# Kernel tuning notes

Measured on AMD Instinct MI355X. Metric: run time of the kernel, lower is better.

The kernel has to match this reference:

```python
import jax, jax.numpy as jnp
import numpy as np

D_MODEL = 512
D_STATE = 128
D_CONV = 4
EXPAND = 2
HEADDIM = 64
D_INNER = EXPAND * D_MODEL            # 1024
NHEADS = D_INNER // HEADDIM           # 16
CONV_DIM = D_INNER + 2 * D_STATE      # 1280
D_IN_PROJ = 2 * D_INNER + 2 * D_STATE + NHEADS  # 2320
EPS = 1e-5


def _mamba2(u, in_w, conv_w, conv_b, A_log, dt_bias, Dp, norm_w, out_w):
    # u: [b, l, d_model]  -- Mamba2 forward (ngroups=1), SSD in exact quadratic form
    b, l, _ = u.shape
    zxbcdt = u @ in_w.T                                   # [b,l,2320]
    z = zxbcdt[..., :D_INNER]
    xBC = zxbcdt[..., D_INNER:D_INNER + CONV_DIM]
    dt = zxbcdt[..., D_INNER + CONV_DIM:]                 # [b,l,nheads]
    # causal depthwise conv1d (kernel 4) + silu
    xp = jnp.pad(xBC, ((0, 0), (D_CONV - 1, 0), (0, 0)))
    conv = sum(xp[:, k:k + l, :] * conv_w[:, k] for k in range(D_CONV))
    xBC = jax.nn.silu(conv + conv_b)
    x = xBC[..., :D_INNER].reshape(b, l, NHEADS, HEADDIM)
    Bm = xBC[..., D_INNER:D_INNER + D_STATE]              # [b,l,d_state]
    Cm = xBC[..., D_INNER + D_STATE:]                     # [b,l,d_state]
    dt = jax.nn.softplus(dt + dt_bias)                    # [b,l,nheads]
    dtA = dt * (-jnp.exp(A_log))                          # [b,l,nheads], negative
    # SSD quadratic (semiseparable) form: L[t,s] = exp(sum_{r=s+1..t} dtA_r), causal
    cs = jnp.cumsum(dtA, axis=1)                          # [b,l,nh]
    seg = cs[:, :, None, :] - cs[:, None, :, :]           # [b,t,s,nh]
    mask = jnp.tril(jnp.ones((l, l), bool))
    L = jnp.exp(jnp.where(mask[None, :, :, None], seg, -jnp.inf))
    G = jnp.einsum('btd,bsd->bts', Cm, Bm)                # C_t . B_s
    dtx = dt[..., None] * x                               # [b,l,nh,hd]
    y = jnp.einsum('btsn,bsnp->btnp', G[..., None] * L, dtx)
    y = (y + x * Dp[:, None]).reshape(b, l, D_INNER)      # D skip
    # gated RMSNorm (norm_before_gate=False): rmsnorm(y * silu(z)) * weight
    y = y * jax.nn.silu(z)
    y = y * jax.lax.rsqrt(jnp.mean(jnp.square(y), -1, keepdims=True) + EPS) * norm_w
    return y @ out_w.T


def _forward(x, h_in_w, h_conv_w, h_conv_b, h_A_log, h_dt_bias, h_D, h_norm_w, h_out_w,
             v_in_w, v_conv_w, v_conv_b, v_A_log, v_dt_bias, v_D, v_norm_w, v_out_w,
             fc_w, fc_b):
    B, H, W, C = x.shape
    hp = (h_in_w, h_conv_w, h_conv_b, h_A_log, h_dt_bias, h_D, h_norm_w, h_out_w)
    vp = (v_in_w, v_conv_w, v_conv_b, v_A_log, v_dt_bias, v_D, v_norm_w, v_out_w)
    # horizontal: scan along W for each (B*H) row
    xh = x.reshape(-1, W, C)
    h1 = _mamba2(xh, *hp)
    # NOTE: original code flips dim 0 (batch), reproduced faithfully
    h2 = jnp.flip(_mamba2(jnp.flip(xh, 0), *hp), 0)
    h = jnp.concatenate([h1, h2], -1).reshape(B, H, W, -1)
    # vertical: scan along H for each (B*W) column
    xv = jnp.transpose(x, (0, 2, 1, 3)).reshape(-1, H, C)
    v1 = _mamba2(xv, *vp)
    v2 = jnp.flip(_mamba2(jnp.flip(xv, 0), *vp), 0)
    v = jnp.transpose(jnp.concatenate([v1, v2], -1).reshape(B, W, H, -1), (0, 2, 1, 3))
    out = jnp.concatenate([v, h], -1) @ fc_w.T + fc_b     # [B,H,W,C]
    return out


def setup_inputs() -> dict:
    key = jax.random.key(0)
    ks = jax.random.split(key, 8)
    B, H, W, C = 2, 64, 64, D_MODEL
    x = jax.random.normal(ks[0], (B, H, W, C), jnp.float32)

    def mk(k):
        kk = jax.random.split(k, 5)
        return {
            'in_w': 0.02 * jax.random.normal(kk[0], (D_IN_PROJ, D_MODEL), jnp.float32),
            'conv_w': 0.1 * jax.random.normal(kk[1], (CONV_DIM, D_CONV), jnp.float32),
            'conv_b': jnp.zeros((CONV_DIM,), jnp.float32),
            'A_log': jnp.log(jax.random.uniform(kk[2], (NHEADS,), jnp.float32, 1.0, 16.0)),
            'dt_bias': jnp.log(jnp.expm1(jax.random.uniform(kk[3], (NHEADS,), jnp.float32, 1e-3, 0.1))),
            'D': jnp.ones((NHEADS,), jnp.float32),
            'norm_w': jnp.ones((D_INNER,), jnp.float32),
            'out_w': 0.02 * jax.random.normal(kk[4], (D_MODEL, D_INNER), jnp.float32),
        }

    hp, vp = mk(ks[1]), mk(ks[2])
    inp = {'x': x}
    inp.update({f'h_{n}': v for n, v in hp.items()})
    inp.update({f'v_{n}': v for n, v in vp.items()})
    inp['fc_w'] = 0.02 * jax.random.normal(ks[3], (D_MODEL, 4 * D_MODEL), jnp.float32)
    inp['fc_b'] = jnp.zeros((D_MODEL,), jnp.float32)
    return inp


def reference(x, h_in_w, h_conv_w, h_conv_b, h_A_log, h_dt_bias, h_D, h_norm_w, h_out_w,
              v_in_w, v_conv_w, v_conv_b, v_A_log, v_dt_bias, v_D, v_norm_w, v_out_w,
              fc_w, fc_b):
    return _forward(x, h_in_w, h_conv_w, h_conv_b, h_A_log, h_dt_bias, h_D, h_norm_w, h_out_w,
                    v_in_w, v_conv_w, v_conv_b, v_A_log, v_dt_bias, v_D, v_norm_w, v_out_w,
                    fc_w, fc_b)
```

## Files before the change

### kernel.cpp

```cpp
#include <hip/hip_runtime.h>

#define NROWS 8192
#define NZX   2304
#define BCS   136
#define XMS   72

#define PB0 4096
#define PB1 (PB0 + 2048)
#define PB2 (PB1 + 2304)
#define PB3 (PB2 + 256)
#define PB4 (PB3 + 512)

typedef __attribute__((ext_vector_type(8))) short bf16x8;
typedef __attribute__((ext_vector_type(4))) float f32x4;

__device__ __forceinline__ float bf2f(unsigned short u) {
    union { unsigned int i; float f; } v; v.i = ((unsigned int)u) << 16; return v.f;
}
__device__ __forceinline__ unsigned short f2bf(float f) {
    union { float f; unsigned int i; } v; v.f = f;
    return (unsigned short)((v.i + 0x8000u) >> 16);
}

__device__ __forceinline__ void async_lds16(const unsigned short* g, unsigned short* l) {
    __builtin_amdgcn_global_load_lds(
        (const __attribute__((address_space(1))) unsigned int*)g,
        (__attribute__((address_space(3))) unsigned int*)l, 16, 0, 0);
}

__global__ __launch_bounds__(256) void prep_kernel(
    const float* __restrict__ x, const float* __restrict__ fcw,
    const float* __restrict__ iw0, const float* __restrict__ iw1,
    const float* __restrict__ ow0, const float* __restrict__ ow1,
    const float* __restrict__ db0, const float* __restrict__ db1,
    const float* __restrict__ al0, const float* __restrict__ al1,
    unsigned short* __restrict__ xbf, unsigned short* __restrict__ wf,
    unsigned short* __restrict__ wbA, unsigned short* __restrict__ wbOT0,
    unsigned short* __restrict__ wbOT1, float* __restrict__ dtbb,
    float* __restrict__ csbb)
{
    __shared__ char sm[37888] __attribute__((aligned(16)));
    const int blk = blockIdx.x, tid = threadIdx.x;
    if (blk < PB0) {
        int i = blk * 256 + tid;
        float4 v = *(const float4*)(x + (size_t)i * 4);
        ushort4 o;
        o.x = f2bf(v.x); o.y = f2bf(v.y); o.z = f2bf(v.z); o.w = f2bf(v.w);
        *(ushort4*)(xbf + (size_t)i * 4) = o;
    } else if (blk < PB1) {
        int idx = (blk - PB0) * 256 + tid;
        int o = idx >> 10, c = idx & 1023;
        int half = c >> 9, cc = c & 511;
        float v = fcw[(size_t)o * 2048 + half * 1024 + cc] +
                  fcw[(size_t)o * 2048 + half * 1024 + 512 + cc];
        wf[idx] = f2bf(v);
    } else if (blk < PB2) {
        int local = blk - PB1;
        int dir = local / 1152;
        int i = (local % 1152) * 256 + tid;
        const float* s = dir ? iw1 : iw0;
        float4 v = *(const float4*)(s + (size_t)i * 4);
        ushort4 o;
        o.x = f2bf(v.x); o.y = f2bf(v.y); o.z = f2bf(v.z); o.w = f2bf(v.w);
        *(ushort4*)(wbA + (size_t)dir * (2304 * 512) + (size_t)i * 4) = o;
    } else if (blk < PB3) {
        float (*T)[65] = (float(*)[65])sm;
        int local = blk - PB2;
        int z = local >> 7, rem = local & 127;
        const float* s = z ? ow1 : ow0;
        unsigned short* d = z ? wbOT1 : wbOT0;
        const int bo = (rem >> 4) * 64, bc = (rem & 15) * 64;
#pragma unroll
        for (int i = 0; i < 16; ++i) {
            int slot = tid + i * 256;
            int r = slot >> 6, c = slot & 63;
            T[r][c] = s[(size_t)(bo + r) * 1024 + bc + c];
        }
        __syncthreads();
#pragma unroll
        for (int i = 0; i < 16; ++i) {
            int slot = tid + i * 256;
            int cr = slot >> 6, oc = slot & 63;
            d[(size_t)(bc + cr) * 512 + bo + oc] = f2bf(T[oc][cr]);
        }
    } else {
        float (*wsm)[512] = (float(*)[512])sm;
        float (*xs)[68]   = (float(*)[68])(sm + 16384);
        float (*dta)[64]  = (float(*)[64])(sm + 16384 + 17408);
        float (*dtt)[64]  = (float(*)[64])(sm + 16384 + 17408 + 2048);
        int local = blk - PB3;
        const int dir = local >> 8, bxl = local & 255;
        const float* in_w = dir ? iw1 : iw0;
        const float* dt_bias = dir ? db1 : db0;
        const float* A_log = dir ? al1 : al0;
        float* dtb = dtbb + (size_t)dir * 131072;
        float* csb = csbb + (size_t)dir * 131072;
        const int seq = bxl >> 1, hq = bxl & 1;
#pragma unroll
        for (int i = 0; i < 4; ++i) {
            int slot = tid + i * 256;
            int h = slot >> 7, c = (slot & 127) * 4;
            *(float4*)&wsm[h][c] = *(const float4*)(in_w + (size_t)(2304 + hq * 8 + h) * 512 + c);
        }
        const int t = tid & 63, hg = tid >> 6;
        float acc[2] = {0.f, 0.f};
        for (int c0 = 0; c0 < 512; c0 += 64) {
            __syncthreads();
#pragma unroll
            for (int i = 0; i < 4; ++i) {
                int slot = tid + i * 256;
                int r = slot >> 4, cc = (slot & 15) * 4;
                size_t row = (dir == 0) ? (size_t)seq * 64 + r
                                        : (size_t)(seq >> 6) * 4096 + (size_t)r * 64 + (seq & 63);
                *(float4*)&xs[r][cc] = *(const float4*)(x + row * 512 + c0 + cc);
            }
            __syncthreads();
#pragma unroll
            for (int cc = 0; cc < 64; cc += 4) {
                float4 u4 = *(const float4*)&xs[t][cc];
                const float* w0 = &wsm[hg * 2][c0 + cc];
                const float* w1 = &wsm[hg * 2 + 1][c0 + cc];
                acc[0] += u4.x * w0[0] + u4.y * w0[1] + u4.z * w0[2] + u4.w * w0[3];
                acc[1] += u4.x * w1[0] + u4.y * w1[1] + u4.z * w1[2] + u4.w * w1[3];
            }
        }
#pragma unroll
        for (int hh = 0; hh < 2; ++hh) {
            int hl = hg * 2 + hh;
            int h = hq * 8 + hl;
            float v = acc[hh] + dt_bias[h];
            float dtv = (v > 20.f) ? v : log1pf(__expf(v));
            dtt[hl][t] = dtv;
            dta[hl][t] = dtv * -__expf(A_log[h]);
        }
        __syncthreads();
        if (tid < 8) {
            float run = 0.f;
            int ob = (seq * 16 + hq * 8 + tid) * 64;
            for (int tt = 0; tt < 64; ++tt) {
                run += dta[tid][tt];
                dtb[ob + tt] = dtt[tid][tt];
                csb[ob + tt] = run;
            }
        }
    }
}

__global__ __launch_bounds__(256) void gemm_phase(
    const unsigned short* __restrict__ xbf, const unsigned short* __restrict__ wbA,
    unsigned short* __restrict__ zx, const unsigned short* __restrict__ wf,
    const unsigned short* __restrict__ wbOT0, const unsigned short* __restrict__ wbOT1,
    unsigned short* __restrict__ wcomb)
{
    __shared__ unsigned short SMEM[16384];
    unsigned short* As = SMEM;
    unsigned short* Bs = SMEM + 8192;
    const int bx = blockIdx.x, by = blockIdx.y, z = blockIdx.z;
    const unsigned short *A, *B;
    unsigned short* C;
    int lda, ldb, ldc, perm, mB, nB;
    if (bx < 64) {
        A = xbf; lda = 512; perm = z;
        B = wbA + (size_t)z * (2304 * 512); ldb = 512;
        C = zx + (size_t)z * NROWS * NZX; ldc = NZX;
        mB = bx * 128; nB = by * 128;
    } else {
        if (by >= 8) return;
        A = z ? wf : wf + 512; lda = 1024; perm = 0;
        B = z ? wbOT1 : wbOT0; ldb = 512;
        C = z ? wcomb : wcomb + 1024; ldc = 2048;
        mB = (bx - 64) * 128; nB = by * 128;
    }
    const int tid = threadIdx.x, wave = tid >> 6, lane = tid & 63;
    const int wm = (wave >> 1) * 64, wn = (wave & 1) * 64;
    const int lr = lane & 15, lq = lane >> 4;
    const unsigned short* AgP[4];
    const unsigned short* BgP[4];
    unsigned short* lA[4];
    unsigned short* lB[4];
#pragma unroll
    for (int i = 0; i < 4; ++i) {
        int s = tid + i * 256;
        int r = s >> 3, p = s & 7;
        int q = p ^ (r & 7);
        int ar = mB + r;
        if (perm) ar = (ar & ~4095) | ((ar & 63) << 6) | ((ar >> 6) & 63);
        AgP[i] = A + (size_t)ar * lda + q * 8;
        BgP[i] = B + (size_t)(nB + r) * ldb + q * 8;
        lA[i] = As + s * 8;
        lB[i] = Bs + s * 8;
    }
    const int aswz = lr & 7;
    int arb[4], brb[4];
#pragma unroll
    for (int i = 0; i < 4; ++i) {
        arb[i] = (wm + i * 16 + lr) * 64;
        brb[i] = (wn + i * 16 + lr) * 64;
    }
    f32x4 zero4 = {0.f,0.f,0.f,0.f};
    f32x4 acc[4][4] = {{zero4,zero4,zero4,zero4},{zero4,zero4,zero4,zero4},
                       {zero4,zero4,zero4,zero4},{zero4,zero4,zero4,zero4}};
    for (int k0 = 0; k0 < 512; k0 += 64) {
#pragma unroll
        for (int i = 0; i < 4; ++i) async_lds16(AgP[i] + k0, lA[i]);
#pragma unroll
        for (int i = 0; i < 4; ++i) async_lds16(BgP[i] + k0, lB[i]);
        __syncthreads();
#pragma unroll
        for (int kh = 0; kh < 2; ++kh) {
            const int ksw = ((kh * 4 + lq) ^ aswz) * 8;
            bf16x8 a[4], b[4];
#pragma unroll
            for (int i = 0; i < 4; ++i) a[i] = *(const bf16x8*)(As + arb[i] + ksw);
#pragma unroll
            for (int i = 0; i < 4; ++i) b[i] = *(const bf16x8*)(Bs + brb[i] + ksw);
#pragma unroll
            for (int mi = 0; mi < 4; ++mi)
#pragma unroll
                for (int ni = 0; ni < 4; ++ni)
                    acc[mi][ni] = __builtin_amdgcn_mfma_f32_16x16x32_bf16(
                        a[mi], b[ni], acc[mi][ni], 0, 0, 0);
        }
        __syncthreads();
    }
    unsigned short* WR = SMEM + wave * 1024;
#pragma unroll
    for (int mi = 0; mi < 4; ++mi) {
#pragma unroll
        for (int ni = 0; ni < 4; ++ni) {
#pragma unroll
            for (int r = 0; r < 4; ++r) {
                int r16 = lq * 4 + r;
                int cn = ni * 16 + lr;
                int gp = ((cn >> 3) + (r16 >> 1)) & 7;
                WR[r16 * 64 + gp * 8 + (cn & 7)] = f2bf(acc[mi][ni][r]);
            }
        }
#pragma unroll
        for (int j = 0; j < 2; ++j) {
            int r16 = j * 8 + (lane >> 3);
            int gr = lane & 7;
            int gp = (gr + (r16 >> 1)) & 7;
            uint4 v = *(const uint4*)(WR + r16 * 64 + gp * 8);
            int row = mB + wm + mi * 16 + r16;
            *(uint4*)(C + (size_t)row * ldc + nB + wn + gr * 8) = v;
        }
    }
}

__global__ __launch_bounds__(256) void gemm_final2048(
    const unsigned short* __restrict__ YV, const unsigned short* __restrict__ YH,
    const unsigned short* __restrict__ W, const float* __restrict__ bias,
    float* __restrict__ C)
{
    __shared__ unsigned short As[128 * 64];
    __shared__ unsigned short Bs[64 * 64];
    const int tid = threadIdx.x, wave = tid >> 6, lane = tid & 63;
    const int mB = blockIdx.x * 128, nB = blockIdx.y * 64;
    const int lr = lane & 15, lq = lane >> 4;
    int aq[4], agr[4], apr[4];
    unsigned short* lA[4];
    const unsigned short* BgP[2];
    unsigned short* lB[2];
#pragma unroll
    for (int i = 0; i < 4; ++i) {
        int s = tid + i * 256;
        int r = s >> 3, p = s & 7;
        aq[i] = (p ^ (r & 7)) * 8;
        int gr = mB + r;
        agr[i] = gr;
        apr[i] = (gr & ~4095) | ((gr & 63) << 6) | ((gr >> 6) & 63);
        lA[i] = As + s * 8;
    }
#pragma unroll
    for (int i = 0; i < 2; ++i) {
        int s = tid + i * 256;
        int r = s >> 3, p = s & 7;
        int q = p ^ (r & 7);
        BgP[i] = W + (size_t)(nB + r) * 2048 + q * 8;
        lB[i] = Bs + s * 8;
    }
    const int aswz = lr & 7;
    int arb[2], brb[4];
#pragma unroll
    for (int i = 0; i < 2; ++i) arb[i] = (wave * 32 + i * 16 + lr) * 64;
#pragma unroll
    for (int i = 0; i < 4; ++i) brb[i] = (i * 16 + lr) * 64;
    f32x4 zero4 = {0.f,0.f,0.f,0.f};
    f32x4 acc[2][4] = {{zero4,zero4,zero4,zero4},{zero4,zero4,zero4,zero4}};
    for (int k0 = 0; k0 < 2048; k0 += 64) {
#pragma unroll
        for (int i = 0; i < 4; ++i) {
            int kk = k0 + aq[i];
            const unsigned short* g = (kk < 1024)
                ? YV + (size_t)apr[i] * 1024 + kk
                : YH + (size_t)agr[i] * 1024 + (kk - 1024);
            async_lds16(g, lA[i]);
        }
#pragma unroll
        for (int i = 0; i < 2; ++i) async_lds16(BgP[i] + k0, lB[i]);
        __syncthreads();
#pragma unroll
        for (int kh = 0; kh < 2; ++kh) {
            const int ksw = ((kh * 4 + lq) ^ aswz) * 8;
            bf16x8 a[2], b[4];
#pragma unroll
            for (int i = 0; i < 2; ++i) a[i] = *(const bf16x8*)(As + arb[i] + ksw);
#pragma unroll
            for (int i = 0; i < 4; ++i) b[i] = *(const bf16x8*)(Bs + brb[i] + ksw);
#pragma unroll
            for (int mi = 0; mi < 2; ++mi)
#pragma unroll
                for (int ni = 0; ni < 4; ++ni)
                    acc[mi][ni] = __builtin_amdgcn_mfma_f32_16x16x32_bf16(
                        a[mi], b[ni], acc[mi][ni], 0, 0, 0);
        }
        __syncthreads();
    }
    const int rbase = lq * 4;
#pragma unroll
    for (int mi = 0; mi < 2; ++mi)
#pragma unroll
        for (int ni = 0; ni < 4; ++ni) {
            int col = nB + ni * 16 + lr;
            float bb = bias[col];
#pragma unroll
            for (int r = 0; r < 4; ++r) {
                int row = mB + wave * 32 + mi * 16 + rbase + r;
                C[(size_t)row * 512 + col] = acc[mi][ni][r] + bb;
            }
        }
}

__global__ __launch_bounds__(320) void conv_silu(
    const unsigned short* __restrict__ zxb, const float* __restrict__ cw0,
    const float* __restrict__ cw1, const float* __restrict__ cb0,
    const float* __restrict__ cb1, unsigned short* __restrict__ xbcb)
{
    __shared__ unsigned short S[64 * 320];
    const int dir = blockIdx.y;
    const unsigned short* zx = zxb + (size_t)dir * NROWS * NZX;
    unsigned short* xbc = xbcb + (size_t)dir * NROWS * 1280;
    const float* cw = dir ? cw1 : cw0;
    const float* cb = dir ? cb1 : cb0;
    const int tid = threadIdx.x;
    const int seq = blockIdx.x >> 2, tile = blockIdx.x & 3;
    const int cbase = tile * 320;
    const unsigned short* src = zx + (size_t)seq * 64 * NZX + 1024 + cbase;
#pragma unroll
    for (int i = 0; i < 8; ++i) {
        int slot = tid + i * 320;
        int r = slot / 40, ch = (slot % 40) * 8;
        *(uint4*)(S + r * 320 + ch) = *(const uint4*)(src + (size_t)r * NZX + ch);
    }
    __syncthreads();
    const int c8 = (tid % 40) * 8, rg = tid / 40;
    const int gc = cbase + c8;
    float4 b0 = *(const float4*)(cb + gc), b1 = *(const float4*)(cb + gc + 4);
    const float bias[8] = {b0.x,b0.y,b0.z,b0.w,b1.x,b1.y,b1.z,b1.w};
    float4 wv[8];
#pragma unroll
    for (int j = 0; j < 8; ++j) wv[j] = *(const float4*)(cw + (size_t)(gc + j) * 4);
    unsigned short* dst = xbc + (size_t)seq * 64 * 1280 + gc;
#pragma unroll
    for (int r = 0; r < 8; ++r) {
        int t = rg * 8 + r;
        float acc[8];
#pragma unroll
        for (int j = 0; j < 8; ++j) acc[j] = bias[j];
#pragma unroll
        for (int k = 0; k < 4; ++k) {
            int ts = t + k - 3;
            if (ts >= 0) {
                uint4 xv = *(const uint4*)(S + ts * 320 + c8);
                const unsigned short* xs = (const unsigned short*)&xv;
#pragma unroll
                for (int j = 0; j < 8; ++j)
                    acc[j] += bf2f(xs[j]) * ((const float*)&wv[j])[k];
            }
        }
        unsigned short out8[8] __attribute__((aligned(16)));
#pragma unroll
        for (int j = 0; j < 8; ++j) out8[j] = f2bf(acc[j] / (1.f + __expf(-acc[j])));
        *(uint4*)(dst + (size_t)t * 1280) = *(const uint4*)out8;
    }
}

__global__ __launch_bounds__(256) void scan_kernel(
    const unsigned short* __restrict__ xbcb, const float* __restrict__ dtbb,
    const float* __restrict__ csbb, const float* __restrict__ Dv0,
    const float* __restrict__ Dv1, unsigned short* __restrict__ yh,
    unsigned short* __restrict__ yv)
{
    __shared__ unsigned short Bs[64 * BCS];
    __shared__ unsigned short Cs[64 * BCS];
    __shared__ unsigned short XsT[64 * XMS];
    __shared__ unsigned short Ms[64 * XMS];
    __shared__ float dts[64], css[64];
    const int dir = blockIdx.y;
    const unsigned short* xbc = xbcb + (size_t)dir * NROWS * 1280;
    const float* dtb = dtbb + (size_t)dir * 131072;
    const float* csb = csbb + (size_t)dir * 131072;
    const float* Dv = dir ? Dv1 : Dv0;
    unsigned short* y = dir ? yv : yh;
    const int tid = threadIdx.x;
    const int lane = tid & 63, wave = tid >> 6;
    const int seq = blockIdx.x >> 4, h = blockIdx.x & 15;
    if (tid < 64) {
        dts[tid] = dtb[(seq * 16 + h) * 64 + tid];
        css[tid] = csb[(seq * 16 + h) * 64 + tid];
    }
    const unsigned short* base = xbc + (size_t)seq * 64 * 1280;
#pragma unroll
    for (int i = 0; i < 4; ++i) {
        int e = (tid + i * 256) * 8;
        int r = e >> 7, c = e & 127;
        *(uint4*)(Bs + r * BCS + c) = *(const uint4*)(base + (size_t)r * 1280 + 1024 + c);
        *(uint4*)(Cs + r * BCS + c) = *(const uint4*)(base + (size_t)r * 1280 + 1152 + c);
    }
#pragma unroll
    for (int i = 0; i < 2; ++i) {
        int e = (tid + i * 256) * 8;
        int t = e >> 6, p0 = e & 63;
        uint4 xval = *(const uint4*)(base + (size_t)t * 1280 + h * 64 + p0);
        const unsigned short* xs = (const unsigned short*)&xval;
#pragma unroll
        for (int j = 0; j < 8; ++j) {
            int jl = (j + lane) & 7;
            XsT[(p0 + jl) * XMS + t] = xs[jl];
        }
    }
    __syncthreads();
    const int lr = lane & 15, lq = lane >> 4;
    f32x4 zero4 = {0.f,0.f,0.f,0.f};
    f32x4 acc[4] = {zero4, zero4, zero4, zero4};
#pragma unroll
    for (int kt = 0; kt < 4; ++kt) {
        bf16x8 a = *(const bf16x8*)(Cs + (wave * 16 + lr) * BCS + kt * 32 + lq * 8);
#pragma unroll
        for (int ni = 0; ni < 4; ++ni) {
            bf16x8 b = *(const bf16x8*)(Bs + (ni * 16 + lr) * BCS + kt * 32 + lq * 8);
            acc[ni] = __builtin_amdgcn_mfma_f32_16x16x32_bf16(a, b, acc[ni], 0, 0, 0);
        }
    }
    float css_t[4];
#pragma unroll
    for (int r = 0; r < 4; ++r) css_t[r] = css[wave * 16 + lq * 4 + r];
#pragma unroll
    for (int ni = 0; ni < 4; ++ni) {
        int s = ni * 16 + lr;
        float cs_s = css[s], dt_s = dts[s];
#pragma unroll
        for (int r = 0; r < 4; ++r) {
            int t = wave * 16 + lq * 4 + r;
            float e = __expf(fminf(css_t[r] - cs_s, 0.f));
            float m = (s <= t) ? acc[ni][r] * e * dt_s : 0.f;
            Ms[t * XMS + s] = f2bf(m);
        }
    }
    __syncthreads();
    f32x4 yacc[4] = {zero4, zero4, zero4, zero4};
#pragma unroll
    for (int kt = 0; kt < 2; ++kt) {
        bf16x8 a = *(const bf16x8*)(Ms + (wave * 16 + lr) * XMS + kt * 32 + lq * 8);
#pragma unroll
        for (int ni = 0; ni < 4; ++ni) {
            bf16x8 b = *(const bf16x8*)(XsT + (ni * 16 + lr) * XMS + kt * 32 + lq * 8);
            yacc[ni] = __builtin_amdgcn_mfma_f32_16x16x32_bf16(a, b, yacc[ni], 0, 0, 0);
        }
    }
    const float Dh = Dv[h];
#pragma unroll
    for (int ni = 0; ni < 4; ++ni) {
        int p = ni * 16 + lr;
#pragma unroll
        for (int r = 0; r < 4; ++r) {
            int t = wave * 16 + lq * 4 + r;
            float v = yacc[ni][r] + Dh * bf2f(XsT[p * XMS + t]);
            Ms[t * XMS + p] = f2bf(v);
        }
    }
    __syncthreads();
    unsigned short* yout = y + (size_t)seq * 64 * 1024 + h * 64;
#pragma unroll
    for (int i = 0; i < 2; ++i) {
        int slot = tid + i * 256;
        int t = slot >> 3, pc = (slot & 7) * 8;
        uint4 v = *(const uint4*)(Ms + t * XMS + pc);
        *(uint4*)(yout + (size_t)t * 1024 + pc) = v;
    }
}

__global__ __launch_bounds__(128) void gate_norm(
    const unsigned short* __restrict__ zxb, unsigned short* __restrict__ yh,
    unsigned short* __restrict__ yv, const float* __restrict__ nw0,
    const float* __restrict__ nw1)
{
    const int dir = blockIdx.y;
    const unsigned short* zx = zxb + (size_t)dir * NROWS * NZX;
    unsigned short* y = dir ? yv : yh;
    const float* nw = dir ? nw1 : nw0;
    const int row = blockIdx.x, tid = threadIdx.x;
    uint4 yv4 = *(const uint4*)(y + (size_t)row * 1024 + tid * 8);
    uint4 zv4 = *(const uint4*)(zx + (size_t)row * NZX + tid * 8);
    const unsigned short* ys = (const unsigned short*)&yv4;
    const unsigned short* zs = (const unsigned short*)&zv4;
    float g[8]; float ss = 0.f;
#pragma unroll
    for (int j = 0; j < 8; ++j) {
        float zv = bf2f(zs[j]);
        float gv = bf2f(ys[j]) * (zv / (1.f + __expf(-zv)));
        g[j] = gv; ss += gv * gv;
    }
#pragma unroll
    for (int off = 32; off > 0; off >>= 1) ss += __shfl_xor(ss, off, 64);
    __shared__ float red[2];
    if ((tid & 63) == 0) red[tid >> 6] = ss;
    __syncthreads();
    ss = red[0] + red[1];
    const float scale = rsqrtf(ss * (1.f / 1024.f) + 1e-5f);
    unsigned short out8[8] __attribute__((aligned(16)));
#pragma unroll
    for (int j = 0; j < 8; ++j) out8[j] = f2bf(g[j] * scale * nw[tid * 8 + j]);
    *(uint4*)(y + (size_t)row * 1024 + tid * 8) = *(const uint4*)out8;
}

extern "C" void kernel_launch(void* const* d_in, const int* in_sizes, int n_in,
                              void* d_out, int out_size, void* d_ws, size_t ws_size,
                              hipStream_t stream)
{
    (void)in_sizes; (void)n_in; (void)out_size; (void)ws_size;
    const float* x   = (const float*)d_in[0];
    const float* fcw = (const float*)d_in[17];
    const float* fcb = (const float*)d_in[18];
    const float* iw0 = (const float*)d_in[1];  const float* iw1 = (const float*)d_in[9];
    const float* cw0 = (const float*)d_in[2];  const float* cw1 = (const float*)d_in[10];
    const float* cb0 = (const float*)d_in[3];  const float* cb1 = (const float*)d_in[11];
    const float* al0 = (const float*)d_in[4];  const float* al1 = (const float*)d_in[12];
    const float* db0 = (const float*)d_in[5];  const float* db1 = (const float*)d_in[13];
    const float* Dv0 = (const float*)d_in[6];  const float* Dv1 = (const float*)d_in[14];
    const float* nw0 = (const float*)d_in[7];  const float* nw1 = (const float*)d_in[15];
    const float* ow0 = (const float*)d_in[8];  const float* ow1 = (const float*)d_in[16];

    char* ws = (char*)d_ws;
    size_t off = 0;
    auto alloc = [&](size_t bytes) {
        void* p = ws + off; off += (bytes + 255) & ~(size_t)255; return p;
    };
    unsigned short* xbf   = (unsigned short*)alloc((size_t)NROWS * 512 * 2);
    unsigned short* wbA   = (unsigned short*)alloc((size_t)2 * 2304 * 512 * 2);
    unsigned short* wbOT0 = (unsigned short*)alloc((size_t)1024 * 512 * 2);
    unsigned short* wbOT1 = (unsigned short*)alloc((size_t)1024 * 512 * 2);
    unsigned short* wf    = (unsigned short*)alloc((size_t)512 * 1024 * 2);
    unsigned short* wcomb = (unsigned short*)alloc((size_t)512 * 2048 * 2);
    unsigned short* zx    = (unsigned short*)alloc((size_t)2 * NROWS * NZX * 2);
    unsigned short* xbc   = (unsigned short*)alloc((size_t)2 * NROWS * 1280 * 2);
    float* dtb            = (float*)alloc((size_t)2 * 2048 * 64 * 4);
    float* csb            = (float*)alloc((size_t)2 * 2048 * 64 * 4);
    unsigned short* ybh   = (unsigned short*)alloc((size_t)NROWS * 1024 * 2);
    unsigned short* ybv   = (unsigned short*)alloc((size_t)NROWS * 1024 * 2);

    prep_kernel<<<PB4, 256, 0, stream>>>(x, fcw, iw0, iw1, ow0, ow1, db0, db1,
                                         al0, al1, xbf, wf, wbA, wbOT0, wbOT1,
                                         dtb, csb);
    gemm_phase<<<dim3(68, 18, 2), 256, 0, stream>>>(xbf, wbA, zx, wf,
                                                    wbOT0, wbOT1, wcomb);
    conv_silu<<<dim3(512, 2), 320, 0, stream>>>(zx, cw0, cw1, cb0, cb1, xbc);
    scan_kernel<<<dim3(2048, 2), 256, 0, stream>>>(xbc, dtb, csb, Dv0, Dv1, ybh, ybv);
    gate_norm<<<dim3(NROWS, 2), 128, 0, stream>>>(zx, ybh, ybv, nw0, nw1);
    gemm_final2048<<<dim3(64, 8), 256, 0, stream>>>(ybv, ybh, wcomb, fcb, (float*)d_out);
}
```

Baseline: 294.1 us.

## Fuse x bf16 conversion into dt prep and process two heads per scan block

The standalone x-to-bf16 conversion blocks in prep_kernel are removed; instead, the dt/cumsum blocks for direction 0 (first head quarter) write bf16 x from their already-staged shared-memory tile, avoiding a second read of x. The scan kernel now handles two heads per block, so the B·C Gram matrix is computed once and reused for both heads. This halves the scan grid and removes redundant Gram MFMAs and B/C loads, at the cost of larger shared memory, more serialized work per block and extra barriers. Block-to-sequence mapping is also swizzled.

Result: slower. 306.5 us (+4.2%).

```diff
diff --git a/kernel.cpp b/kernel.cpp
--- a/kernel.cpp
+++ b/kernel.cpp
@@ -5,11 +5,10 @@
 #define BCS   136
 #define XMS   72
 
-#define PB0 4096
-#define PB1 (PB0 + 2048)
-#define PB2 (PB1 + 2304)
-#define PB3 (PB2 + 256)
-#define PB4 (PB3 + 512)
+#define PB0 2048
+#define PB1 (PB0 + 2304)
+#define PB2 (PB1 + 256)
+#define PB3 (PB2 + 512)
 
 typedef __attribute__((ext_vector_type(8))) short bf16x8;
 typedef __attribute__((ext_vector_type(4))) float f32x4;
@@ -42,20 +41,14 @@
     __shared__ char sm[37888] __attribute__((aligned(16)));
     const int blk = blockIdx.x, tid = threadIdx.x;
     if (blk < PB0) {
-        int i = blk * 256 + tid;
-        float4 v = *(const float4*)(x + (size_t)i * 4);
-        ushort4 o;
-        o.x = f2bf(v.x); o.y = f2bf(v.y); o.z = f2bf(v.z); o.w = f2bf(v.w);
-        *(ushort4*)(xbf + (size_t)i * 4) = o;
-    } else if (blk < PB1) {
-        int idx = (blk - PB0) * 256 + tid;
+        int idx = blk * 256 + tid;
         int o = idx >> 10, c = idx & 1023;
         int half = c >> 9, cc = c & 511;
         float v = fcw[(size_t)o * 2048 + half * 1024 + cc] +
                   fcw[(size_t)o * 2048 + half * 1024 + 512 + cc];
         wf[idx] = f2bf(v);
-    } else if (blk < PB2) {
-        int local = blk - PB1;
+    } else if (blk < PB1) {
+        int local = blk - PB0;
         int dir = local / 1152;
         int i = (local % 1152) * 256 + tid;
         const float* s = dir ? iw1 : iw0;
@@ -63,9 +56,9 @@
         ushort4 o;
         o.x = f2bf(v.x); o.y = f2bf(v.y); o.z = f2bf(v.z); o.w = f2bf(v.w);
         *(ushort4*)(wbA + (size_t)dir * (2304 * 512) + (size_t)i * 4) = o;
-    } else if (blk < PB3) {
+    } else if (blk < PB2) {
         float (*T)[65] = (float(*)[65])sm;
-        int local = blk - PB2;
+        int local = blk - PB1;
         int z = local >> 7, rem = local & 127;
         const float* s = z ? ow1 : ow0;
         unsigned short* d = z ? wbOT1 : wbOT0;
@@ -88,7 +81,7 @@
         float (*xs)[68]   = (float(*)[68])(sm + 16384);
         float (*dta)[64]  = (float(*)[64])(sm + 16384 + 17408);
         float (*dtt)[64]  = (float(*)[64])(sm + 16384 + 17408 + 2048);
-        int local = blk - PB3;
+        int local = blk - PB2;
         const int dir = local >> 8, bxl = local & 255;
         const float* in_w = dir ? iw1 : iw0;
         const float* dt_bias = dir ? db1 : db0;
@@ -96,6 +89,7 @@
         float* dtb = dtbb + (size_t)dir * 131072;
         float* csb = csbb + (size_t)dir * 131072;
         const int seq = bxl >> 1, hq = bxl & 1;
+        const bool emit_x = (dir == 0) && (hq == 0);
 #pragma unroll
         for (int i = 0; i < 4; ++i) {
             int slot = tid + i * 256;
@@ -115,6 +109,18 @@
                 *(float4*)&xs[r][cc] = *(const float4*)(x + row * 512 + c0 + cc);
             }
             __syncthreads();
+            if (emit_x) {
+#pragma unroll
+                for (int i = 0; i < 2; ++i) {
+                    int slot = tid + i * 256;
+                    int r = slot >> 3, cc8 = (slot & 7) * 8;
+                    unsigned short o8[8] __attribute__((aligned(16)));
+#pragma unroll
+                    for (int j = 0; j < 8; ++j) o8[j] = f2bf(xs[r][cc8 + j]);
+                    *(uint4*)(xbf + (size_t)(seq * 64 + r) * 512 + c0 + cc8) =
+                        *(const uint4*)o8;
+                }
+            }
 #pragma unroll
             for (int cc = 0; cc < 64; cc += 4) {
                 float4 u4 = *(const float4*)&xs[t][cc];
@@ -394,9 +400,9 @@
 {
     __shared__ unsigned short Bs[64 * BCS];
     __shared__ unsigned short Cs[64 * BCS];
-    __shared__ unsigned short XsT[64 * XMS];
+    __shared__ unsigned short XsT[2][64 * XMS];
     __shared__ unsigned short Ms[64 * XMS];
-    __shared__ float dts[64], css[64];
+    __shared__ float dts[2][64], css[2][64];
     const int dir = blockIdx.y;
     const unsigned short* xbc = xbcb + (size_t)dir * NROWS * 1280;
     const float* dtb = dtbb + (size_t)dir * 131072;
@@ -405,10 +411,13 @@
     unsigned short* y = dir ? yv : yh;
     const int tid = threadIdx.x;
     const int lane = tid & 63, wave = tid >> 6;
-    const int seq = blockIdx.x >> 4, h = blockIdx.x & 15;
-    if (tid < 64) {
-        dts[tid] = dtb[(seq * 16 + h) * 64 + tid];
-        css[tid] = csb[(seq * 16 + h) * 64 + tid];
+    const int bxr = blockIdx.x;
+    const int seq = (bxr & 7) | ((bxr >> 6) << 3);
+    const int hp = (bxr >> 3) & 7;
+    if (tid < 128) {
+        int hh = tid >> 6, t = tid & 63;
+        dts[hh][t] = dtb[(seq * 16 + hp * 2 + hh) * 64 + t];
+        css[hh][t] = csb[(seq * 16 + hp * 2 + hh) * 64 + t];
     }
     const unsigned short* base = xbc + (size_t)seq * 64 * 1280;
 #pragma unroll
@@ -419,15 +428,16 @@
         *(uint4*)(Cs + r * BCS + c) = *(const uint4*)(base + (size_t)r * 1280 + 1152 + c);
     }
 #pragma unroll
-    for (int i = 0; i < 2; ++i) {
+    for (int i = 0; i < 4; ++i) {
         int e = (tid + i * 256) * 8;
-        int t = e >> 6, p0 = e & 63;
-        uint4 xval = *(const uint4*)(base + (size_t)t * 1280 + h * 64 + p0);
-        const unsigned short* xs = (const unsigned short*)&xval;
+        int t = e >> 7, c0 = e & 127;
+        int hh = c0 >> 6, p0 = c0 & 63;
+        uint4 xval = *(const uint4*)(base + (size_t)t * 1280 + hp * 128 + c0);
+        const unsigned short* xsv = (const unsigned short*)&xval;
 #pragma unroll
         for (int j = 0; j < 8; ++j) {
             int jl = (j + lane) & 7;
-            XsT[(p0 + jl) * XMS + t] = xs[jl];
+            XsT[hh][(p0 + jl) * XMS + t] = xsv[jl];
         }
     }
     __syncthreads();
@@ -443,51 +453,55 @@
             acc[ni] = __builtin_amdgcn_mfma_f32_16x16x32_bf16(a, b, acc[ni], 0, 0, 0);
         }
     }
-    float css_t[4];
-#pragma unroll
-    for (int r = 0; r < 4; ++r) css_t[r] = css[wave * 16 + lq * 4 + r];
-#pragma unroll
-    for (int ni = 0; ni < 4; ++ni) {
-        int s = ni * 16 + lr;
-        float cs_s = css[s], dt_s = dts[s];
-#pragma unroll
-        for (int r = 0; r < 4; ++r) {
-            int t = wave * 16 + lq * 4 + r;
-            float e = __expf(fminf(css_t[r] - cs_s, 0.f));
-            float m = (s <= t) ? acc[ni][r] * e * dt_s : 0.f;
-            Ms[t * XMS + s] = f2bf(m);
-        }
-    }
-    __syncthreads();
-    f32x4 yacc[4] = {zero4, zero4, zero4, zero4};
-#pragma unroll
-    for (int kt = 0; kt < 2; ++kt) {
-        bf16x8 a = *(const bf16x8*)(Ms + (wave * 16 + lr) * XMS + kt * 32 + lq * 8);
+    for (int hh = 0; hh < 2; ++hh) {
+        float css_t[4];
+#pragma unroll
+        for (int r = 0; r < 4; ++r) css_t[r] = css[hh][wave * 16 + lq * 4 + r];
 #pragma unroll
         for (int ni = 0; ni < 4; ++ni) {
-            bf16x8 b = *(const bf16x8*)(XsT + (ni * 16 + lr) * XMS + kt * 32 + lq * 8);
-            yacc[ni] = __builtin_amdgcn_mfma_f32_16x16x32_bf16(a, b, yacc[ni], 0, 0, 0);
-        }
-    }
-    const float Dh = Dv[h];
-#pragma unroll
-    for (int ni = 0; ni < 4; ++ni) {
-        int p = ni * 16 + lr;
-#pragma unroll
-        for (int r = 0; r < 4; ++r) {
-            int t = wave * 16 + lq * 4 + r;
-            float v = yacc[ni][r] + Dh * bf2f(XsT[p * XMS + t]);
-            Ms[t * XMS + p] = f2bf(v);
-        }
-    }
-    __syncthreads();
-    unsigned short* yout = y + (size_t)seq * 64 * 1024 + h * 64;
-#pragma unroll
-    for (int i = 0; i < 2; ++i) {
-        int slot = tid + i * 256;
-        int t = slot >> 3, pc = (slot & 7) * 8;
-        uint4 v = *(const uint4*)(Ms + t * XMS + pc);
-        *(uint4*)(yout + (size_t)t * 1024 + pc) = v;
+            int s = ni * 16 + lr;
+            float cs_s = css[hh][s], dt_s = dts[hh][s];
+#pragma unroll
+            for (int r = 0; r < 4; ++r) {
+                int t = wave * 16 + lq * 4 + r;
+                float e = __expf(fminf(css_t[r] - cs_s, 0.f));
+                float m = (s <= t) ? acc[ni][r] * e * dt_s : 0.f;
+                Ms[t * XMS + s] = f2bf(m);
+            }
+        }
+        __syncthreads();
+        f32x4 yacc[4] = {zero4, zero4, zero4, zero4};
+#pragma unroll
+        for (int kt = 0; kt < 2; ++kt) {
+            bf16x8 a = *(const bf16x8*)(Ms + (wave * 16 + lr) * XMS + kt * 32 + lq * 8);
+#pragma unroll
+            for (int ni = 0; ni < 4; ++ni) {
+                bf16x8 b = *(const bf16x8*)(XsT[hh] + (ni * 16 + lr) * XMS + kt * 32 + lq * 8);
+                yacc[ni] = __builtin_amdgcn_mfma_f32_16x16x32_bf16(a, b, yacc[ni], 0, 0, 0);
+            }
+        }
+        __syncthreads();
+        const float Dh = Dv[hp * 2 + hh];
+#pragma unroll
+        for (int ni = 0; ni < 4; ++ni) {
+            int p = ni * 16 + lr;
+#pragma unroll
+            for (int r = 0; r < 4; ++r) {
+                int t = wave * 16 + lq * 4 + r;
+                float v = yacc[ni][r] + Dh * bf2f(XsT[hh][p * XMS + t]);
+                Ms[t * XMS + p] = f2bf(v);
+            }
+        }
+        __syncthreads();
+        unsigned short* yout = y + (size_t)seq * 64 * 1024 + (hp * 2 + hh) * 64;
+#pragma unroll
+        for (int i = 0; i < 2; ++i) {
+            int slot = tid + i * 256;
+            int t = slot >> 3, pc = (slot & 7) * 8;
+            uint4 v = *(const uint4*)(Ms + t * XMS + pc);
+            *(uint4*)(yout + (size_t)t * 1024 + pc) = v;
+        }
+        __syncthreads();
     }
 }
 
@@ -560,13 +574,13 @@
     unsigned short* ybh   = (unsigned short*)alloc((size_t)NROWS * 1024 * 2);
     unsigned short* ybv   = (unsigned short*)alloc((size_t)NROWS * 1024 * 2);
 
-    prep_kernel<<<PB4, 256, 0, stream>>>(x, fcw, iw0, iw1, ow0, ow1, db0, db1,
+    prep_kernel<<<PB3, 256, 0, stream>>>(x, fcw, iw0, iw1, ow0, ow1, db0, db1,
                                          al0, al1, xbf, wf, wbA, wbOT0, wbOT1,
                                          dtb, csb);
     gemm_phase<<<dim3(68, 18, 2), 256, 0, stream>>>(xbf, wbA, zx, wf,
                                                     wbOT0, wbOT1, wcomb);
     conv_silu<<<dim3(512, 2), 320, 0, stream>>>(zx, cw0, cw1, cb0, cb1, xbc);
-    scan_kernel<<<dim3(2048, 2), 256, 0, stream>>>(xbc, dtb, csb, Dv0, Dv1, ybh, ybv);
+    scan_kernel<<<dim3(1024, 2), 256, 0, stream>>>(xbc, dtb, csb, Dv0, Dv1, ybh, ybv);
     gate_norm<<<dim3(NROWS, 2), 128, 0, stream>>>(zx, ybh, ybv, nw0, nw1);
     gemm_final2048<<<dim3(64, 8), 256, 0, stream>>>(ybv, ybh, wcomb, fcb, (float*)d_out);
 }
```

## Compute C·B^T Gram matrix once per sequence and share it across heads

Applied to the files above, without the earlier changes.

The C·B^T product per 64-token sequence was recomputed in all 16 per-head scan blocks. A new gmat_kernel computes it once per sequence and direction into an fp32 global buffer, and scan_kernel now reads it back instead of loading B/C and running MFMAs. This removes 16x redundant loads and matrix math and cuts scan LDS use. In exchange it adds an extra launch, a 4 MB fp32 round trip, and strided uncoalesced global reads of G in the scan.

New measurement: 289.9 us. Within noise of the previous version (-1.5%).

```diff
diff --git a/kernel.cpp b/kernel.cpp
--- a/kernel.cpp
+++ b/kernel.cpp
@@ -386,14 +386,54 @@
     }
 }
 
-__global__ __launch_bounds__(256) void scan_kernel(
-    const unsigned short* __restrict__ xbcb, const float* __restrict__ dtbb,
-    const float* __restrict__ csbb, const float* __restrict__ Dv0,
-    const float* __restrict__ Dv1, unsigned short* __restrict__ yh,
-    unsigned short* __restrict__ yv)
+__global__ __launch_bounds__(256) void gmat_kernel(
+    const unsigned short* __restrict__ xbcb, float* __restrict__ Gbuf)
 {
     __shared__ unsigned short Bs[64 * BCS];
     __shared__ unsigned short Cs[64 * BCS];
+    const int dir = blockIdx.y, seq = blockIdx.x;
+    const unsigned short* base = xbcb + (size_t)dir * NROWS * 1280
+                                      + (size_t)seq * 64 * 1280;
+    const int tid = threadIdx.x;
+    const int lane = tid & 63, wave = tid >> 6;
+#pragma unroll
+    for (int i = 0; i < 4; ++i) {
+        int e = (tid + i * 256) * 8;
+        int r = e >> 7, c = e & 127;
+        *(uint4*)(Bs + r * BCS + c) = *(const uint4*)(base + (size_t)r * 1280 + 1024 + c);
+        *(uint4*)(Cs + r * BCS + c) = *(const uint4*)(base + (size_t)r * 1280 + 1152 + c);
+    }
+    __syncthreads();
+    const int lr = lane & 15, lq = lane >> 4;
+    f32x4 zero4 = {0.f,0.f,0.f,0.f};
+    f32x4 acc[4] = {zero4, zero4, zero4, zero4};
+#pragma unroll
+    for (int kt = 0; kt < 4; ++kt) {
+        bf16x8 a = *(const bf16x8*)(Cs + (wave * 16 + lr) * BCS + kt * 32 + lq * 8);
+#pragma unroll
+        for (int ni = 0; ni < 4; ++ni) {
+            bf16x8 b = *(const bf16x8*)(Bs + (ni * 16 + lr) * BCS + kt * 32 + lq * 8);
+            acc[ni] = __builtin_amdgcn_mfma_f32_16x16x32_bf16(a, b, acc[ni], 0, 0, 0);
+        }
+    }
+    float* G = Gbuf + ((size_t)dir * 128 + seq) * 4096;
+#pragma unroll
+    for (int ni = 0; ni < 4; ++ni) {
+        int s = ni * 16 + lr;
+#pragma unroll
+        for (int r = 0; r < 4; ++r) {
+            int t = wave * 16 + lq * 4 + r;
+            G[t * 64 + s] = acc[ni][r];
+        }
+    }
+}
+
+__global__ __launch_bounds__(256) void scan_kernel(
+    const unsigned short* __restrict__ xbcb, const float* __restrict__ Gbuf,
+    const float* __restrict__ dtbb, const float* __restrict__ csbb,
+    const float* __restrict__ Dv0, const float* __restrict__ Dv1,
+    unsigned short* __restrict__ yh, unsigned short* __restrict__ yv)
+{
     __shared__ unsigned short XsT[64 * XMS];
     __shared__ unsigned short Ms[64 * XMS];
     __shared__ float dts[64], css[64];
@@ -412,13 +452,6 @@
     }
     const unsigned short* base = xbc + (size_t)seq * 64 * 1280;
 #pragma unroll
-    for (int i = 0; i < 4; ++i) {
-        int e = (tid + i * 256) * 8;
-        int r = e >> 7, c = e & 127;
-        *(uint4*)(Bs + r * BCS + c) = *(const uint4*)(base + (size_t)r * 1280 + 1024 + c);
-        *(uint4*)(Cs + r * BCS + c) = *(const uint4*)(base + (size_t)r * 1280 + 1152 + c);
-    }
-#pragma unroll
     for (int i = 0; i < 2; ++i) {
         int e = (tid + i * 256) * 8;
         int t = e >> 6, p0 = e & 63;
@@ -430,19 +463,19 @@
             XsT[(p0 + jl) * XMS + t] = xs[jl];
         }
     }
+    const int lr = lane & 15, lq = lane >> 4;
+    const float* G = Gbuf + ((size_t)dir * 128 + seq) * 4096;
+    f32x4 acc[4];
+#pragma unroll
+    for (int ni = 0; ni < 4; ++ni) {
+        int s = ni * 16 + lr;
+#pragma unroll
+        for (int r = 0; r < 4; ++r) {
+            int t = wave * 16 + lq * 4 + r;
+            acc[ni][r] = G[t * 64 + s];
+        }
+    }
     __syncthreads();
-    const int lr = lane & 15, lq = lane >> 4;
-    f32x4 zero4 = {0.f,0.f,0.f,0.f};
-    f32x4 acc[4] = {zero4, zero4, zero4, zero4};
-#pragma unroll
-    for (int kt = 0; kt < 4; ++kt) {
-        bf16x8 a = *(const bf16x8*)(Cs + (wave * 16 + lr) * BCS + kt * 32 + lq * 8);
-#pragma unroll
-        for (int ni = 0; ni < 4; ++ni) {
-            bf16x8 b = *(const bf16x8*)(Bs + (ni * 16 + lr) * BCS + kt * 32 + lq * 8);
-            acc[ni] = __builtin_amdgcn_mfma_f32_16x16x32_bf16(a, b, acc[ni], 0, 0, 0);
-        }
-    }
     float css_t[4];
 #pragma unroll
     for (int r = 0; r < 4; ++r) css_t[r] = css[wave * 16 + lq * 4 + r];
@@ -459,6 +492,7 @@
         }
     }
     __syncthreads();
+    f32x4 zero4 = {0.f,0.f,0.f,0.f};
     f32x4 yacc[4] = {zero4, zero4, zero4, zero4};
 #pragma unroll
     for (int kt = 0; kt < 2; ++kt) {
@@ -555,6 +589,7 @@
     unsigned short* wcomb = (unsigned short*)alloc((size_t)512 * 2048 * 2);
     unsigned short* zx    = (unsigned short*)alloc((size_t)2 * NROWS * NZX * 2);
     unsigned short* xbc   = (unsigned short*)alloc((size_t)2 * NROWS * 1280 * 2);
+    float* Gbuf           = (float*)alloc((size_t)2 * 128 * 4096 * 4);
     float* dtb            = (float*)alloc((size_t)2 * 2048 * 64 * 4);
     float* csb            = (float*)alloc((size_t)2 * 2048 * 64 * 4);
     unsigned short* ybh   = (unsigned short*)alloc((size_t)NROWS * 1024 * 2);
@@ -566,7 +601,9 @@
     gemm_phase<<<dim3(68, 18, 2), 256, 0, stream>>>(xbf, wbA, zx, wf,
                                                     wbOT0, wbOT1, wcomb);
     conv_silu<<<dim3(512, 2), 320, 0, stream>>>(zx, cw0, cw1, cb0, cb1, xbc);
-    scan_kernel<<<dim3(2048, 2), 256, 0, stream>>>(xbc, dtb, csb, Dv0, Dv1, ybh, ybv);
+    gmat_kernel<<<dim3(128, 2), 256, 0, stream>>>(xbc, Gbuf);
+    scan_kernel<<<dim3(2048, 2), 256, 0, stream>>>(xbc, Gbuf, dtb, csb,
+                                                   Dv0, Dv1, ybh, ybv);
     gate_norm<<<dim3(NROWS, 2), 128, 0, stream>>>(zx, ybh, ybv, nw0, nw1);
     gemm_final2048<<<dim3(64, 8), 256, 0, stream>>>(ybv, ybh, wcomb, fcb, (float*)d_out);
 }
```
